# Performance work log

Measured on AMD Instinct MI355X. Metric: run time of the kernel, lower is better.

Reference implementation:

```python
import jax, jax.numpy as jnp
import numpy as np

N_CLASSES = 8
EPS = 1e-5


def setup_inputs() -> dict:
    key = jax.random.key(0)
    k1, k2, k3, k4 = jax.random.split(key, 4)
    B, F, L = 512, 128, 1024
    x = jax.random.normal(k1, (B, F, L), dtype=jnp.float32)
    labels = jax.random.randint(k2, (B,), 0, N_CLASSES, dtype=jnp.int32)
    weight = jax.random.normal(k3, (N_CLASSES, F), dtype=jnp.float32)
    bias = jax.random.normal(k4, (N_CLASSES, F), dtype=jnp.float32)
    return {"x": x, "labels": labels, "weight": weight, "bias": bias}


def reference(x, labels, weight, bias):
    # x: [B, F, L]; labels: [B] in [0, n_classes); weight/bias: [K, F]
    # Per-class training-mode BatchNorm1d: biased mean/var over the class's
    # (batch_subset, length) elements per feature, then per-class affine.
    B, F, L = x.shape
    mask = jax.nn.one_hot(labels, N_CLASSES, dtype=x.dtype)      # [B, K]
    cnt = jnp.maximum(mask.sum(axis=0) * L, 1.0)                  # [K] elements per class
    sum_x = jnp.einsum('bk,bfl->kf', mask, x)                     # [K, F]
    sum_x2 = jnp.einsum('bk,bfl->kf', mask, x * x)                # [K, F]
    mean = sum_x / cnt[:, None]                                   # [K, F]
    var = sum_x2 / cnt[:, None] - mean * mean                     # biased variance
    inv = jax.lax.rsqrt(var + EPS)                                # [K, F]
    scale = (inv * weight)[labels][:, :, None]                    # [B, F, 1]
    shift = (bias - mean * inv * weight)[labels][:, :, None]      # [B, F, 1]
    return x * scale + shift
```

## Files before the change

### kernel.cpp

```cpp
#include <hip/hip_runtime.h>

#define B_DIM 512
#define F_DIM 128
#define L_DIM 1024
#define K_CLS 8
#define EPS 1e-5f
#define NROWS (B_DIM * F_DIM)

typedef float vf4 __attribute__((ext_vector_type(4)));

#define WS_S2    (K_CLS * F_DIM)
#define WS_SCALE (2 * K_CLS * F_DIM)
#define WS_SHIFT (3 * K_CLS * F_DIM)

__global__ __launch_bounds__(256) void cbn_stats(const float* __restrict__ x,
                                                 const int* __restrict__ labels,
                                                 float* __restrict__ ws) {
    const int wave = threadIdx.x >> 6;
    const int lane = threadIdx.x & 63;
    const int row  = blockIdx.x * 4 + wave;
    const int b = row >> 7;
    const int f = row & (F_DIM - 1);

    const vf4* x4 = reinterpret_cast<const vf4*>(x) + (size_t)row * (L_DIM / 4);

    float s = 0.f, s2 = 0.f;
#pragma unroll
    for (int i = 0; i < 4; ++i) {
        vf4 v = x4[i * 64 + lane];
        s  += v.x + v.y + v.z + v.w;
        s2 += v.x * v.x + v.y * v.y + v.z * v.z + v.w * v.w;
    }
#pragma unroll
    for (int m = 32; m >= 1; m >>= 1) {
        s  += __shfl_xor(s, m);
        s2 += __shfl_xor(s2, m);
    }
    if (lane == 0) {
        const int k = labels[b];
        atomicAdd(&ws[k * F_DIM + f], s);
        atomicAdd(&ws[WS_S2 + k * F_DIM + f], s2);
    }
}

__global__ __launch_bounds__(1024) void cbn_finalize(const int* __restrict__ labels,
                                                     const float* __restrict__ weight,
                                                     const float* __restrict__ bias,
                                                     float* __restrict__ ws) {
    __shared__ int cnt[K_CLS];
    const int t = threadIdx.x;
    if (t < K_CLS) cnt[t] = 0;
    __syncthreads();
    if (t < B_DIM) atomicAdd(&cnt[labels[t]], 1);
    __syncthreads();

    const int k = t >> 7;
    const float c = fmaxf((float)cnt[k] * (float)L_DIM, 1.0f);
    const float sum   = ws[t];
    const float sumsq = ws[WS_S2 + t];
    const float mean = sum / c;
    const float var  = sumsq / c - mean * mean;
    const float inv  = rsqrtf(var + EPS);
    const float sc   = inv * weight[t];
    ws[WS_SCALE + t] = sc;
    ws[WS_SHIFT + t] = bias[t] - mean * sc;
}

#define APPLY_ROWS 4
__global__ __launch_bounds__(256) void cbn_apply(const float* __restrict__ x,
                                                 const int* __restrict__ labels,
                                                 const float* __restrict__ ws,
                                                 float* __restrict__ y) {
    const int nBlocks = NROWS / APPLY_ROWS;
    const int blk = nBlocks - 1 - blockIdx.x;
    const int row0 = blk * APPLY_ROWS;

#pragma unroll
    for (int it = 0; it < APPLY_ROWS; ++it) {
        const int row = row0 + it;
        const int b = row >> 7;
        const int f = row & (F_DIM - 1);
        const int k = labels[b];
        const float sc = ws[WS_SCALE + k * F_DIM + f];
        const float sh = ws[WS_SHIFT + k * F_DIM + f];

        const size_t i4 = (size_t)row * (L_DIM / 4) + threadIdx.x;
        vf4 v = reinterpret_cast<const vf4*>(x)[i4];
        vf4 o;
        o.x = v.x * sc + sh;
        o.y = v.y * sc + sh;
        o.z = v.z * sc + sh;
        o.w = v.w * sc + sh;
        __builtin_nontemporal_store(o, &reinterpret_cast<vf4*>(y)[i4]);
    }
}

extern "C" void kernel_launch(void* const* d_in, const int* in_sizes, int n_in,
                              void* d_out, int out_size, void* d_ws, size_t ws_size,
                              hipStream_t stream) {
    const float* x      = (const float*)d_in[0];
    const int*   labels = (const int*)d_in[1];
    const float* weight = (const float*)d_in[2];
    const float* bias   = (const float*)d_in[3];
    float* y  = (float*)d_out;
    float* ws = (float*)d_ws;

    hipMemsetAsync(ws, 0, 2 * K_CLS * F_DIM * sizeof(float), stream);

    cbn_stats<<<NROWS / 4, 256, 0, stream>>>(x, labels, ws);
    cbn_finalize<<<1, 1024, 0, stream>>>(labels, weight, bias, ws);
    cbn_apply<<<NROWS / APPLY_ROWS, 256, 0, stream>>>(x, labels, ws, y);
}
```

Measured before the change: 133.4 us.

## Fuse stats, finalize and apply into one cooperative persistent kernel

Replaces the memset plus three kernel launches with a single cooperative kernel of 1024 blocks that computes per-row sums, syncs the grid, reduces per-feature class statistics without global atomics, syncs again, and applies the affine transform. Each block handles the same 64 rows in both passes, so the second read of x may hit in the large last-level cache. It also removes the launch gaps between stages. In exchange it adds two grid-wide barriers and relies on cooperative launch residency, and only 128 blocks are busy during finalize.

```diff
diff --git a/kernel.cpp b/kernel.cpp
--- a/kernel.cpp
+++ b/kernel.cpp
@@ -1,4 +1,7 @@
 #include <hip/hip_runtime.h>
+#include <hip/hip_cooperative_groups.h>
+
+namespace cg = cooperative_groups;
 
 #define B_DIM 512
 #define F_DIM 128
@@ -6,85 +9,85 @@
 #define K_CLS 8
 #define EPS 1e-5f
 #define NROWS (B_DIM * F_DIM)
+#define GRID  1024
+#define RPB   (NROWS / GRID)
 
 typedef float vf4 __attribute__((ext_vector_type(4)));
 
-#define WS_S2    (K_CLS * F_DIM)
-#define WS_SCALE (2 * K_CLS * F_DIM)
-#define WS_SHIFT (3 * K_CLS * F_DIM)
+#define ST_SQ    NROWS
+#define ST_SCALE (2 * NROWS)
+#define ST_SHIFT (2 * NROWS + K_CLS * F_DIM)
 
-__global__ __launch_bounds__(256) void cbn_stats(const float* __restrict__ x,
-                                                 const int* __restrict__ labels,
-                                                 float* __restrict__ ws) {
-    const int wave = threadIdx.x >> 6;
-    const int lane = threadIdx.x & 63;
-    const int row  = blockIdx.x * 4 + wave;
-    const int b = row >> 7;
-    const int f = row & (F_DIM - 1);
+__global__ __launch_bounds__(256, 4) void cbn_fused(const float* __restrict__ x,
+                                                    const int* __restrict__ labels,
+                                                    const float* __restrict__ weight,
+                                                    const float* __restrict__ bias,
+                                                    float* __restrict__ st,
+                                                    float* __restrict__ y) {
+    const int blk  = blockIdx.x;
+    const int tid  = threadIdx.x;
+    const int wave = tid >> 6;
+    const int lane = tid & 63;
+    const int r0   = blk * RPB;
 
-    const vf4* x4 = reinterpret_cast<const vf4*>(x) + (size_t)row * (L_DIM / 4);
+    for (int i = 0; i < RPB / 4; ++i) {
+        const int row = r0 + wave * (RPB / 4) + i;
+        const vf4* x4 = reinterpret_cast<const vf4*>(x) + (size_t)row * (L_DIM / 4);
+        float s = 0.f, s2 = 0.f;
+#pragma unroll
+        for (int j = 0; j < 4; ++j) {
+            vf4 v = x4[j * 64 + lane];
+            s  += v.x + v.y + v.z + v.w;
+            s2 += v.x * v.x + v.y * v.y + v.z * v.z + v.w * v.w;
+        }
+#pragma unroll
+        for (int m = 32; m >= 1; m >>= 1) {
+            s  += __shfl_xor(s, m);
+            s2 += __shfl_xor(s2, m);
+        }
+        if (lane == 0) {
+            const int b = row >> 7;
+            const int f = row & (F_DIM - 1);
+            st[f * B_DIM + b]         = s;
+            st[ST_SQ + f * B_DIM + b] = s2;
+        }
+    }
+    cg::this_grid().sync();
 
-    float s = 0.f, s2 = 0.f;
-#pragma unroll
-    for (int i = 0; i < 4; ++i) {
-        vf4 v = x4[i * 64 + lane];
-        s  += v.x + v.y + v.z + v.w;
-        s2 += v.x * v.x + v.y * v.y + v.z * v.z + v.w * v.w;
+    if (blk < F_DIM) {
+        __shared__ float ssum[K_CLS], ssq[K_CLS];
+        __shared__ int   cnt[K_CLS];
+        if (tid < K_CLS) { ssum[tid] = 0.f; ssq[tid] = 0.f; cnt[tid] = 0; }
+        __syncthreads();
+        const int f = blk;
+        for (int b = tid; b < B_DIM; b += 256) {
+            const int k = labels[b];
+            atomicAdd(&ssum[k], st[f * B_DIM + b]);
+            atomicAdd(&ssq[k],  st[ST_SQ + f * B_DIM + b]);
+            atomicAdd(&cnt[k], 1);
+        }
+        __syncthreads();
+        if (tid < K_CLS) {
+            const float c    = fmaxf((float)cnt[tid] * (float)L_DIM, 1.0f);
+            const float mean = ssum[tid] / c;
+            const float var  = ssq[tid] / c - mean * mean;
+            const float inv  = rsqrtf(var + EPS);
+            const float sc   = inv * weight[tid * F_DIM + f];
+            st[ST_SCALE + tid * F_DIM + f] = sc;
+            st[ST_SHIFT + tid * F_DIM + f] = bias[tid * F_DIM + f] - mean * sc;
+        }
     }
-#pragma unroll
-    for (int m = 32; m >= 1; m >>= 1) {
-        s  += __shfl_xor(s, m);
-        s2 += __shfl_xor(s2, m);
-    }
-    if (lane == 0) {
-        const int k = labels[b];
-        atomicAdd(&ws[k * F_DIM + f], s);
-        atomicAdd(&ws[WS_S2 + k * F_DIM + f], s2);
-    }
-}
+    cg::this_grid().sync();
 
-__global__ __launch_bounds__(1024) void cbn_finalize(const int* __restrict__ labels,
-                                                     const float* __restrict__ weight,
-                                                     const float* __restrict__ bias,
-                                                     float* __restrict__ ws) {
-    __shared__ int cnt[K_CLS];
-    const int t = threadIdx.x;
-    if (t < K_CLS) cnt[t] = 0;
-    __syncthreads();
-    if (t < B_DIM) atomicAdd(&cnt[labels[t]], 1);
-    __syncthreads();
-
-    const int k = t >> 7;
-    const float c = fmaxf((float)cnt[k] * (float)L_DIM, 1.0f);
-    const float sum   = ws[t];
-    const float sumsq = ws[WS_S2 + t];
-    const float mean = sum / c;
-    const float var  = sumsq / c - mean * mean;
-    const float inv  = rsqrtf(var + EPS);
-    const float sc   = inv * weight[t];
-    ws[WS_SCALE + t] = sc;
-    ws[WS_SHIFT + t] = bias[t] - mean * sc;
-}
-
-#define APPLY_ROWS 4
-__global__ __launch_bounds__(256) void cbn_apply(const float* __restrict__ x,
-                                                 const int* __restrict__ labels,
-                                                 const float* __restrict__ ws,
-                                                 float* __restrict__ y) {
-    const int nBlocks = NROWS / APPLY_ROWS;
-    const int blk = nBlocks - 1 - blockIdx.x;
-    const int row0 = blk * APPLY_ROWS;
-
-#pragma unroll
-    for (int it = 0; it < APPLY_ROWS; ++it) {
-        const int row = row0 + it;
-        const int b = row >> 7;
+    const int b = r0 >> 7;
+    const int k = labels[b];
+#pragma unroll 4
+    for (int it = 0; it < RPB; ++it) {
+        const int row = r0 + it;
         const int f = row & (F_DIM - 1);
-        const int k = labels[b];
-        const float sc = ws[WS_SCALE + k * F_DIM + f];
-        const float sh = ws[WS_SHIFT + k * F_DIM + f];
-
-        const size_t i4 = (size_t)row * (L_DIM / 4) + threadIdx.x;
+        const float sc = st[ST_SCALE + k * F_DIM + f];
+        const float sh = st[ST_SHIFT + k * F_DIM + f];
+        const size_t i4 = (size_t)row * (L_DIM / 4) + tid;
         vf4 v = reinterpret_cast<const vf4*>(x)[i4];
         vf4 o;
         o.x = v.x * sc + sh;
@@ -103,11 +106,10 @@
     const float* weight = (const float*)d_in[2];
     const float* bias   = (const float*)d_in[3];
     float* y  = (float*)d_out;
-    float* ws = (float*)d_ws;
+    float* st = (float*)d_ws;
 
-    hipMemsetAsync(ws, 0, 2 * K_CLS * F_DIM * sizeof(float), stream);
-
-    cbn_stats<<<NROWS / 4, 256, 0, stream>>>(x, labels, ws);
-    cbn_finalize<<<1, 1024, 0, stream>>>(labels, weight, bias, ws);
-    cbn_apply<<<NROWS / APPLY_ROWS, 256, 0, stream>>>(x, labels, ws, y);
+    void* args[] = { (void*)&x, (void*)&labels, (void*)&weight, (void*)&bias,
+                     (void*)&st, (void*)&y };
+    hipLaunchCooperativeKernel((const void*)cbn_fused, dim3(GRID), dim3(256),
+                               args, 0, stream);
 }
```

Result: slower. 351.5 us (+163.4%).

## Fuse per-class finalize into apply kernel and process 32 rows per block

Applied to the files above, without the earlier changes.

Removes the single-block finalize kernel and recomputes scale/shift inside each apply block, using a block-level class count over labels and shared memory for 32 rows' coefficients. Each apply block now handles 32 rows instead of 4. This drops one kernel launch and its serialization point. In exchange every block redundantly re-reads labels and recomputes statistics, and the grid has fewer, larger blocks.

```diff
diff --git a/kernel.cpp b/kernel.cpp
--- a/kernel.cpp
+++ b/kernel.cpp
@@ -9,13 +9,11 @@
 
 typedef float vf4 __attribute__((ext_vector_type(4)));
 
-#define WS_S2    (K_CLS * F_DIM)
-#define WS_SCALE (2 * K_CLS * F_DIM)
-#define WS_SHIFT (3 * K_CLS * F_DIM)
+#define ST_SQ (K_CLS * F_DIM)
 
 __global__ __launch_bounds__(256) void cbn_stats(const float* __restrict__ x,
                                                  const int* __restrict__ labels,
-                                                 float* __restrict__ ws) {
+                                                 float* __restrict__ stats) {
     const int wave = threadIdx.x >> 6;
     const int lane = threadIdx.x & 63;
     const int row  = blockIdx.x * 4 + wave;
@@ -38,53 +36,55 @@
     }
     if (lane == 0) {
         const int k = labels[b];
-        atomicAdd(&ws[k * F_DIM + f], s);
-        atomicAdd(&ws[WS_S2 + k * F_DIM + f], s2);
+        atomicAdd(&stats[k * F_DIM + f], s);
+        atomicAdd(&stats[ST_SQ + k * F_DIM + f], s2);
     }
 }
 
-__global__ __launch_bounds__(1024) void cbn_finalize(const int* __restrict__ labels,
-                                                     const float* __restrict__ weight,
-                                                     const float* __restrict__ bias,
-                                                     float* __restrict__ ws) {
-    __shared__ int cnt[K_CLS];
-    const int t = threadIdx.x;
-    if (t < K_CLS) cnt[t] = 0;
+#define RPB 32
+__global__ __launch_bounds__(256) void cbn_final_apply(const float* __restrict__ x,
+                                                       const int* __restrict__ labels,
+                                                       const float* __restrict__ weight,
+                                                       const float* __restrict__ bias,
+                                                       const float* __restrict__ stats,
+                                                       float* __restrict__ y) {
+    const int tid = threadIdx.x;
+    const int nBlocks = NROWS / RPB;
+    const int blk = nBlocks - 1 - blockIdx.x;
+    const int r0 = blk * RPB;
+    const int b0 = r0 >> 7;
+    const int f0 = r0 & (F_DIM - 1);
+    const int k  = labels[b0];
+
+    __shared__ int   s_cnt;
+    __shared__ float s_sc[RPB], s_sh[RPB];
+    if (tid == 0) s_cnt = 0;
     __syncthreads();
-    if (t < B_DIM) atomicAdd(&cnt[labels[t]], 1);
+    {
+        int c = (labels[tid] == k) + (labels[tid + 256] == k);
+#pragma unroll
+        for (int m = 32; m >= 1; m >>= 1) c += __shfl_xor(c, m);
+        if ((tid & 63) == 0) atomicAdd(&s_cnt, c);
+    }
+    __syncthreads();
+    if (tid < RPB) {
+        const int f = f0 + tid;
+        const float cnt  = fmaxf((float)s_cnt * (float)L_DIM, 1.0f);
+        const float mean = stats[k * F_DIM + f] / cnt;
+        const float var  = stats[ST_SQ + k * F_DIM + f] / cnt - mean * mean;
+        const float inv  = rsqrtf(var + EPS);
+        const float sc   = inv * weight[k * F_DIM + f];
+        s_sc[tid] = sc;
+        s_sh[tid] = bias[k * F_DIM + f] - mean * sc;
+    }
     __syncthreads();
 
-    const int k = t >> 7;
-    const float c = fmaxf((float)cnt[k] * (float)L_DIM, 1.0f);
-    const float sum   = ws[t];
-    const float sumsq = ws[WS_S2 + t];
-    const float mean = sum / c;
-    const float var  = sumsq / c - mean * mean;
-    const float inv  = rsqrtf(var + EPS);
-    const float sc   = inv * weight[t];
-    ws[WS_SCALE + t] = sc;
-    ws[WS_SHIFT + t] = bias[t] - mean * sc;
-}
-
-#define APPLY_ROWS 4
-__global__ __launch_bounds__(256) void cbn_apply(const float* __restrict__ x,
-                                                 const int* __restrict__ labels,
-                                                 const float* __restrict__ ws,
-                                                 float* __restrict__ y) {
-    const int nBlocks = NROWS / APPLY_ROWS;
-    const int blk = nBlocks - 1 - blockIdx.x;
-    const int row0 = blk * APPLY_ROWS;
-
-#pragma unroll
-    for (int it = 0; it < APPLY_ROWS; ++it) {
-        const int row = row0 + it;
-        const int b = row >> 7;
-        const int f = row & (F_DIM - 1);
-        const int k = labels[b];
-        const float sc = ws[WS_SCALE + k * F_DIM + f];
-        const float sh = ws[WS_SHIFT + k * F_DIM + f];
-
-        const size_t i4 = (size_t)row * (L_DIM / 4) + threadIdx.x;
+#pragma unroll 8
+    for (int it = 0; it < RPB; ++it) {
+        const int row = r0 + it;
+        const float sc = s_sc[it];
+        const float sh = s_sh[it];
+        const size_t i4 = (size_t)row * (L_DIM / 4) + tid;
         vf4 v = reinterpret_cast<const vf4*>(x)[i4];
         vf4 o;
         o.x = v.x * sc + sh;
@@ -102,12 +102,10 @@
     const int*   labels = (const int*)d_in[1];
     const float* weight = (const float*)d_in[2];
     const float* bias   = (const float*)d_in[3];
-    float* y  = (float*)d_out;
-    float* ws = (float*)d_ws;
+    float* y     = (float*)d_out;
+    float* stats = (float*)d_ws;
 
-    hipMemsetAsync(ws, 0, 2 * K_CLS * F_DIM * sizeof(float), stream);
-
-    cbn_stats<<<NROWS / 4, 256, 0, stream>>>(x, labels, ws);
-    cbn_finalize<<<1, 1024, 0, stream>>>(labels, weight, bias, ws);
-    cbn_apply<<<NROWS / APPLY_ROWS, 256, 0, stream>>>(x, labels, ws, y);
+    hipMemsetAsync(stats, 0, 2 * K_CLS * F_DIM * sizeof(float), stream);
+    cbn_stats<<<NROWS / 4, 256, 0, stream>>>(x, labels, stats);
+    cbn_final_apply<<<NROWS / RPB, 256, 0, stream>>>(x, labels, weight, bias, stats, y);
 }
```

Measured after the change: 134.0 us. No clear change (+0.4%).
